# Kernel optimization log

Measured on AMD Instinct MI355X. Metric: run time of the kernel, lower is better.

The kernel has to match this reference:

```python
import jax, jax.numpy as jnp
import numpy as np

B = 16384          # batch
D = 1024           # input_size == hidden size of each block
L = 3              # number of hidden blocks (layer_configs)
H, Q = 4, 64       # num_heads, query_size
NKV, V = 128, 256  # num_key_values, value_size  (H*V == D for residual)
OUT = 256          # out_size
EPS = 1e-5


def layernorm(x, g, b):
    m = jnp.mean(x, axis=-1, keepdims=True)
    v = jnp.mean(jnp.square(x - m), axis=-1, keepdims=True)
    return (x - m) * jax.lax.rsqrt(v + EPS) * g + b


def setup_inputs() -> dict:
    key = jax.random.key(0)
    ks = jax.random.split(key, 16)
    scale = 1e-4  # module scales Linear / out_linear weights by 0.0001 at init
    return {
        "x": jax.random.normal(ks[0], (B, D), jnp.float32),
        # per-block Linear (stacked over L identical blocks)
        "W": jax.random.normal(ks[1], (L, D, D), jnp.float32) * scale / np.sqrt(D),
        "b": jax.random.normal(ks[2], (L, D), jnp.float32) * scale,
        # MemLayer params
        "Wq": jax.random.normal(ks[3], (L, H * Q, D), jnp.float32) / np.sqrt(D),
        "keys": jax.random.normal(ks[4], (L, NKV, Q), jnp.float32),
        "values": jax.random.normal(ks[5], (L, NKV, V), jnp.float32),
        "Wout": jax.random.normal(ks[6], (L, D, H * V), jnp.float32) * scale / np.sqrt(H * V),
        # per-block LayerNorm
        "ln_g": jnp.ones((L, D), jnp.float32),
        "ln_b": jnp.zeros((L, D), jnp.float32),
        # final head: Linear(sum(layer_configs)=L*D -> OUT), LayerNorm, Sigmoid
        "Wf": jax.random.normal(ks[7], (OUT, L * D), jnp.float32) * scale / np.sqrt(L * D),
        "bf": jax.random.normal(ks[8], (OUT,), jnp.float32) * scale,
        "lnf_g": jnp.ones((OUT,), jnp.float32),
        "lnf_b": jnp.zeros((OUT,), jnp.float32),
    }


def reference(x, W, b, Wq, keys, values, Wout, ln_g, ln_b, Wf, bf, lnf_g, lnf_b):
    # Dropout layers are identity at inference.
    inv_sqrt_q = 1.0 / np.sqrt(Q).astype(np.float32)
    outs = []
    h = x
    for i in range(L):
        # Linear + ReLU
        h = jax.nn.relu(h @ W[i].T + b[i])
        # MemLayer: scores = einsum('aib,ajb->aijb').sum(-1) == q @ k^T
        q = (h @ Wq[i].T).reshape(B, H, Q)
        scores = jnp.einsum('ahq,nq->ahn', q, keys[i]) * inv_sqrt_q  # (B,H,NKV)
        attn = jax.nn.softmax(scores, axis=-1)
        # einsum('aib,ajc->aijc').mean(axis=2) == attn.sum(-1)[:,:,None] * values.mean(0)
        s = jnp.sum(attn, axis=-1)              # (B,H)
        vmean = jnp.mean(values[i], axis=0)     # (V,)
        mem = (s[:, :, None] * vmean).reshape(B, H * V)
        h = mem @ Wout[i].T + h                 # out_linear + residual
        # LayerNorm (output collected for the final concat)
        h = layernorm(h, ln_g[i], ln_b[i])
        outs.append(h)
    z = jnp.concatenate(outs, axis=-1)          # (B, L*D)
    z = z @ Wf.T + bf
    z = layernorm(z, lnf_g, lnf_b)
    return jax.nn.sigmoid(z)
```

## Files before the change

### kernel.cpp

```cpp
#include <hip/hip_runtime.h>
#include <math.h>

#define EPS 1e-5f

constexpr int Bv   = 16384;
constexpr int Dv   = 1024;
constexpr int Lv   = 3;
constexpr int NKVv = 128;
constexpr int Vv   = 256;
constexpr int OUTv = 256;
constexpr int ZLD  = Lv * Dv;

typedef short bf16x8 __attribute__((ext_vector_type(8)));
typedef float f32x4  __attribute__((ext_vector_type(4)));

using gas_t = __attribute__((address_space(1))) const void;
using las_t = __attribute__((address_space(3))) void;
#define GLD_LDS16(gp, lp) \
    __builtin_amdgcn_global_load_lds((gas_t*)(gp), (las_t*)(lp), 16, 0, 0)

static __device__ __forceinline__ ushort f2bf(float f) {
    unsigned u = __float_as_uint(f);
    u = (u + 0x7fffu + ((u >> 16) & 1u)) >> 16;
    return (ushort)u;
}
static __device__ __forceinline__ ushort f2h(float f) {
    return __builtin_bit_cast(ushort, (_Float16)f);
}
static __device__ __forceinline__ float h2f(ushort u) {
    return (float)__builtin_bit_cast(_Float16, u);
}

__global__ void vmean_kernel(const float* __restrict__ values,
                             float* __restrict__ vmean) {
    const int i = blockIdx.x, t = threadIdx.x;
    const float* vals = values + (size_t)i * NKVv * Vv;
    float s = 0.f;
    for (int n = 0; n < NKVv; ++n) s += vals[n * Vv + t];
    vmean[i * Vv + t] = s * (1.0f / NKVv);
}

__global__ void cvec_kernel(const float* __restrict__ vmean,
                            const float* __restrict__ Wout,
                            float* __restrict__ cvec) {
    const int w = threadIdx.x >> 6, lane = threadIdx.x & 63;
    const int r = blockIdx.x * 8 + w;
    const int i = r >> 10;
    const float4 mv = *(const float4*)&vmean[i * Vv + lane * 4];
    const float* row = Wout + (size_t)r * 1024;
    float acc = 0.f;
#pragma unroll
    for (int c = 0; c < 4; ++c) {
        const float4 rv = *(const float4*)&row[c * 256 + lane * 4];
        acc += mv.x * rv.x + mv.y * rv.y + mv.z * rv.z + mv.w * rv.w;
    }
#pragma unroll
    for (int o = 1; o < 64; o <<= 1) acc += __shfl_xor(acc, o, 64);
    if (lane == 0) cvec[r] = acc;
}

__global__ void wprep(const float* __restrict__ W,
                      const float* __restrict__ lng,
                      const float* __restrict__ lnb,
                      ushort* __restrict__ Wb,
                      float* __restrict__ ub, float* __restrict__ vb) {
    __shared__ float rs[8];
    const int row = blockIdx.x;
    const int i = row >> 10, n = row & 1023;
    const int t = threadIdx.x, lane = t & 63, wv = t >> 6;
    const float* Wr = W + (size_t)row * 1024;
    const float4 w4 = *(const float4*)&Wr[t * 4];
    float4 g4 = make_float4(1.f, 1.f, 1.f, 1.f);
    float4 b4 = make_float4(0.f, 0.f, 0.f, 0.f);
    if (i > 0) {
        g4 = *(const float4*)&lng[(i - 1) * 1024 + t * 4];
        b4 = *(const float4*)&lnb[(i - 1) * 1024 + t * 4];
    }
    const float s0 = w4.x * g4.x, s1 = w4.y * g4.y, s2 = w4.z * g4.z, s3 = w4.w * g4.w;
    ushort4 o = {f2bf(s0), f2bf(s1), f2bf(s2), f2bf(s3)};
    *(ushort4*)&Wb[(size_t)row * 1024 + t * 4] = o;
    float su = s0 + s1 + s2 + s3;
    float sv = w4.x * b4.x + w4.y * b4.y + w4.z * b4.z + w4.w * b4.w;
#pragma unroll
    for (int d = 1; d < 64; d <<= 1) {
        su += __shfl_xor(su, d, 64);
        sv += __shfl_xor(sv, d, 64);
    }
    if (lane == 0) { rs[wv * 2] = su; rs[wv * 2 + 1] = sv; }
    __syncthreads();
    if (t == 0 && i > 0) {
        ub[(i - 1) * 1024 + n] = rs[0] + rs[2] + rs[4] + rs[6];
        vb[(i - 1) * 1024 + n] = rs[1] + rs[3] + rs[5] + rs[7];
    }
}

__global__ void wfprep(const float* __restrict__ Wf,
                       const float* __restrict__ lng,
                       const float* __restrict__ lnb,
                       ushort* __restrict__ Wfb,
                       float* __restrict__ uf, float* __restrict__ vf) {
    __shared__ float rs[8];
    const int bid = blockIdx.x;
    const int i = bid >> 8, n = bid & 255;
    const int t = threadIdx.x, lane = t & 63, wv = t >> 6;
    const size_t base = (size_t)n * ZLD + i * 1024 + t * 4;
    const float4 w4 = *(const float4*)&Wf[base];
    const float4 g4 = *(const float4*)&lng[i * 1024 + t * 4];
    const float4 b4 = *(const float4*)&lnb[i * 1024 + t * 4];
    const float s0 = w4.x * g4.x, s1 = w4.y * g4.y, s2 = w4.z * g4.z, s3 = w4.w * g4.w;
    ushort4 o = {f2bf(s0), f2bf(s1), f2bf(s2), f2bf(s3)};
    *(ushort4*)&Wfb[base] = o;
    float su = s0 + s1 + s2 + s3;
    float sv = w4.x * b4.x + w4.y * b4.y + w4.z * b4.z + w4.w * b4.w;
#pragma unroll
    for (int d = 1; d < 64; d <<= 1) {
        su += __shfl_xor(su, d, 64);
        sv += __shfl_xor(sv, d, 64);
    }
    if (lane == 0) { rs[wv * 2] = su; rs[wv * 2 + 1] = sv; }
    __syncthreads();
    if (t == 0) {
        uf[i * 256 + n] = rs[0] + rs[2] + rs[4] + rs[6];
        vf[i * 256 + n] = rs[1] + rs[3] + rs[5] + rs[7];
    }
}

__global__ void conv_x(const float* __restrict__ x, ushort* __restrict__ z) {
    const int t = blockIdx.x * 256 + threadIdx.x;
    const int row = t >> 7, c8 = (t & 127) << 3;
    const float4 v0 = *(const float4*)&x[(size_t)row * 1024 + c8];
    const float4 v1 = *(const float4*)&x[(size_t)row * 1024 + c8 + 4];
    ushort4 o0 = {f2bf(v0.x), f2bf(v0.y), f2bf(v0.z), f2bf(v0.w)};
    ushort4 o1 = {f2bf(v1.x), f2bf(v1.y), f2bf(v1.z), f2bf(v1.w)};
    ushort* p = z + (size_t)row * ZLD + 2048 + c8;
    *(ushort4*)p       = o0;
    *(ushort4*)(p + 4) = o1;
}

#define READ_A(QR, DD)                                                        \
    do { _Pragma("unroll")                                                    \
        for (int mf = 0; mf < 4; ++mf) {                                      \
            const int _o = (DD) * 16384 + (QR) * 8192 + (arow_l + mf * 16) * 64; \
            aR[mf][0] = *(const bf16x8*)&As[_o + ck0];                        \
            aR[mf][1] = *(const bf16x8*)&As[_o + ck1];                        \
        } } while (0)

#define READ_B(QC, DD, BR)                                                    \
    do { _Pragma("unroll")                                                    \
        for (int nf = 0; nf < 2; ++nf) {                                      \
            const int _o = (DD) * 16384 + (QC) * 8192 + (brow_l + nf * 16) * 64; \
            BR[nf][0] = *(const bf16x8*)&Bs[_o + ck0];                        \
            BR[nf][1] = *(const bf16x8*)&Bs[_o + ck1];                        \
        } } while (0)

#define STAGE_A(KT, H, DD)                                                    \
    do { const ushort* _p = gAs + (size_t)((H) * 128 + w16) * lda + (KT) * 64; \
         ushort* _l = As + (DD) * 16384 + (H) * 8192 + w16 * 64;              \
         GLD_LDS16(_p, _l);                                                   \
         GLD_LDS16(_p + (size_t)8 * lda, _l + 512); } while (0)

#define STAGE_B(KT, H, DD)                                                    \
    do { const ushort* _p = gBs + (size_t)((H) * 128 + w16) * ldb + (KT) * 64; \
         ushort* _l = Bs + (DD) * 16384 + (H) * 8192 + w16 * 64;              \
         GLD_LDS16(_p, _l);                                                   \
         GLD_LDS16(_p + (size_t)8 * ldb, _l + 512); } while (0)

#define MFMA_Q(QR, QC, BR)                                                    \
    do { __builtin_amdgcn_s_setprio(1);                                       \
        _Pragma("unroll")                                                     \
        for (int mf = 0; mf < 4; ++mf) {                                      \
            _Pragma("unroll")                                                 \
            for (int nf = 0; nf < 2; ++nf) {                                  \
                acc[QR][QC][mf][nf] = __builtin_amdgcn_mfma_f32_16x16x32_bf16( \
                    aR[mf][0], BR[nf][0], acc[QR][QC][mf][nf], 0, 0, 0);      \
                acc[QR][QC][mf][nf] = __builtin_amdgcn_mfma_f32_16x16x32_bf16( \
                    aR[mf][1], BR[nf][1], acc[QR][QC][mf][nf], 0, 0, 0);      \
            }                                                                 \
        }                                                                     \
        __builtin_amdgcn_s_setprio(0); } while (0)

template<int MODE>
__global__ __launch_bounds__(512, 1)
void gemm256(const ushort* __restrict__ A, int lda,
             const ushort* __restrict__ Bw, int ldb,
             const float* __restrict__ bias,
             const float* __restrict__ cvec,
             const float* __restrict__ u_,
             const float* __restrict__ v_,
             const float2* __restrict__ pstats_in,
             float2* __restrict__ mrout,
             void* __restrict__ Cv, int ldc,
             int NT, int ksplit,
             float2* __restrict__ pstats_out) {
    __shared__ __align__(16) char smem[139264];
    ushort* As = (ushort*)smem;
    ushort* Bs = (ushort*)(smem + 65536);
    float2* mrs = (float2*)(smem + 137216);
    const int tid  = threadIdx.x;
    const int lane = tid & 63;
    const int w    = tid >> 6;
    const int wr2  = w >> 2, wc2 = w & 3;
    const int w16  = w * 16;

    const int wg  = blockIdx.x;
    const int qchunk = (MODE == 1) ? 24 : 32;
    const int swz = (wg & 7) * qchunk + (wg >> 3);
    const int by  = swz & 63;
    const int bx  = swz >> 6;
    const int m0  = by * 256;
    const int n0  = (MODE == 1) ? 0 : bx * 256;
    const int koff = (MODE == 1) ? bx * ksplit : 0;

    const int swzc = ((lane & 7) ^ ((lane >> 3) & 7)) << 3;
    const ushort* gAs = A  + (size_t)(m0 + (lane >> 3)) * lda + koff + swzc;
    const ushort* gBs = Bw + (size_t)(n0 + (lane >> 3)) * ldb + koff + swzc;

    const int arow_l = wr2 * 64 + (lane & 15);
    const int brow_l = wc2 * 32 + (lane & 15);
    const int ck0 = (((lane >> 4))     ^ (lane & 7)) << 3;
    const int ck1 = ((4 + (lane >> 4)) ^ (lane & 7)) << 3;

    f32x4 acc[2][2][4][2] = {};
    bf16x8 aR[4][2], bR0[2][2], bR1[2][2];

    const bool doMR = (MODE == 2) || (MODE == 1 && bx == 2);
    float2 myMR = make_float2(0.f, 0.f);
    if (doMR && tid < 256) {
        const float4* pp = (const float4*)(pstats_in + (((size_t)(m0 + tid)) << 4));
        float sum = 0.f, sq = 0.f;
#pragma unroll
        for (int j = 0; j < 8; ++j) {
            const float4 t4 = pp[j];
            sum += t4.x + t4.z; sq += t4.y + t4.w;
        }
        const float m = sum * (1.f / Dv);
        const float var = sq * (1.f / Dv) - m * m;
        myMR = make_float2(m, rsqrtf(var + EPS));
        if (MODE == 2) mrs[tid] = myMR;
    }
    __builtin_amdgcn_sched_barrier(0);

    STAGE_A(0, 0, 0);
    STAGE_B(0, 0, 0);
    STAGE_B(0, 1, 0);
    STAGE_A(0, 1, 0);
    asm volatile("s_waitcnt vmcnt(4)" ::: "memory");
    __builtin_amdgcn_s_barrier();

    for (int t = 0; t < NT; ++t) {
        const int d  = t & 1;
        const int e2 = d ^ 1;
        const bool pf = (t + 1) < NT;
        READ_A(0, d);
        READ_B(0, d, bR0);
        if (pf) STAGE_A(t + 1, 0, e2);
        if (pf) asm volatile("s_waitcnt vmcnt(4)" ::: "memory");
        else    asm volatile("s_waitcnt vmcnt(2)" ::: "memory");
        __builtin_amdgcn_s_barrier();
        MFMA_Q(0, 0, bR0);
        READ_B(1, d, bR1);
        if (pf) STAGE_B(t + 1, 0, e2);
        if (pf) asm volatile("s_waitcnt vmcnt(4)" ::: "memory");
        else    asm volatile("s_waitcnt vmcnt(0)" ::: "memory");
        __builtin_amdgcn_s_barrier();
        MFMA_Q(0, 1, bR1);
        READ_A(1, d);
        if (pf) STAGE_B(t + 1, 1, e2);
        MFMA_Q(1, 1, bR1);
        if (pf) STAGE_A(t + 1, 1, e2);
        if (pf) asm volatile("s_waitcnt vmcnt(4)" ::: "memory");
        __builtin_amdgcn_s_barrier();
        MFMA_Q(1, 0, bR0);
    }

    if (doMR && tid < 256 && (MODE == 1 || bx == 0)) mrout[m0 + tid] = myMR;

    const int lg4 = (lane >> 4) << 2;
    ushort* tile = (ushort*)(smem + 2048);
    if (MODE != 1) {
        float bsv[2][2], csv[2][2], uu[2][2], vv[2][2];
#pragma unroll
        for (int qc = 0; qc < 2; ++qc)
#pragma unroll
            for (int nf = 0; nf < 2; ++nf) {
                const int col = n0 + qc * 128 + wc2 * 32 + nf * 16 + (lane & 15);
                bsv[qc][nf] = bias[col];
                csv[qc][nf] = cvec[col];
                if (MODE == 2) { uu[qc][nf] = u_[col]; vv[qc][nf] = v_[col]; }
            }
        __syncthreads();
#pragma unroll
        for (int qr = 0; qr < 2; ++qr)
#pragma unroll
            for (int mf = 0; mf < 4; ++mf)
#pragma unroll
                for (int r = 0; r < 4; ++r) {
                    const int rloc = qr * 128 + wr2 * 64 + mf * 16 + lg4 + r;
                    float rw = 1.f, rmw = 0.f;
                    if (MODE == 2) {
                        const float2 q = mrs[rloc];
                        rw = q.y; rmw = q.y * q.x;
                    }
                    float sum = 0.f, sq = 0.f;
#pragma unroll
                    for (int qc = 0; qc < 2; ++qc)
#pragma unroll
                        for (int nf = 0; nf < 2; ++nf) {
                            float a = acc[qr][qc][mf][nf][r];
                            float val;
                            if (MODE == 2)
                                val = fmaf(rw, a, fmaf(-rmw, uu[qc][nf],
                                          vv[qc][nf] + bsv[qc][nf]));
                            else
                                val = a + bsv[qc][nf];
                            val = fmaxf(val, 0.f) + csv[qc][nf];
                            acc[qr][qc][mf][nf][r] = val;
                            sum += val; sq += val * val;
                        }
#pragma unroll
                    for (int o = 1; o < 16; o <<= 1) {
                        sum += __shfl_xor(sum, o, 64);
                        sq  += __shfl_xor(sq,  o, 64);
                    }
                    if ((lane & 15) == 0)
                        pstats_out[(((size_t)(m0 + rloc)) << 4) + (bx << 2) + wc2] =
                            make_float2(sum, sq);
                }
#pragma unroll
        for (int qr = 0; qr < 2; ++qr)
#pragma unroll
            for (int qc = 0; qc < 2; ++qc)
#pragma unroll
                for (int mf = 0; mf < 4; ++mf)
#pragma unroll
                    for (int nf = 0; nf < 2; ++nf)
#pragma unroll
                        for (int r = 0; r < 4; ++r) {
                            const int rloc = qr * 128 + wr2 * 64 + mf * 16 + lg4 + r;
                            const int cloc = qc * 128 + wc2 * 32 + nf * 16 + (lane & 15);
                            tile[rloc * 264 + cloc] = f2bf(acc[qr][qc][mf][nf][r]);
                        }
    } else {
        __syncthreads();
#pragma unroll
        for (int qr = 0; qr < 2; ++qr)
#pragma unroll
            for (int qc = 0; qc < 2; ++qc)
#pragma unroll
                for (int mf = 0; mf < 4; ++mf)
#pragma unroll
                    for (int nf = 0; nf < 2; ++nf)
#pragma unroll
                        for (int r = 0; r < 4; ++r) {
                            const int rloc = qr * 128 + wr2 * 64 + mf * 16 + lg4 + r;
                            const int cloc = qc * 128 + wc2 * 32 + nf * 16 + (lane & 15);
                            tile[rloc * 264 + cloc] = f2h(acc[qr][qc][mf][nf][r]);
                        }
    }
    __syncthreads();
    ushort* C16 = (MODE == 1)
        ? ((ushort*)Cv + (size_t)bx * ((size_t)Bv * OUTv))
        : (ushort*)Cv;
    for (int c = tid; c < 256 * 32; c += 512) {
        const int row = c >> 5, ch = (c & 31) << 3;
        const bf16x8 v = *(const bf16x8*)&tile[row * 264 + ch];
        *(bf16x8*)&C16[(size_t)(m0 + row) * ldc + n0 + ch] = v;
    }
}

__global__ void ln_sig_reduce(const ushort* __restrict__ ps,
                              const float2* __restrict__ mr,
                              const float* __restrict__ uf,
                              const float* __restrict__ vf,
                              const float* __restrict__ bf_,
                              const float* __restrict__ g,
                              const float* __restrict__ bb,
                              float* __restrict__ y) {
    const int lane = threadIdx.x & 63;
    const int row  = blockIdx.x * 4 + (threadIdx.x >> 6);
    const size_t base = (size_t)row * OUTv + lane * 4;
    const size_t SP = (size_t)Bv * OUTv;
    const float2 q0 = mr[row];
    const float2 q1 = mr[Bv + row];
    const float2 q2 = mr[2 * Bv + row];
    const ushort4 a0 = *(const ushort4*)&ps[base];
    const ushort4 a1 = *(const ushort4*)&ps[base + SP];
    const ushort4 a2 = *(const ushort4*)&ps[base + 2 * SP];
    const float4 u0 = *(const float4*)&uf[lane * 4];
    const float4 u1 = *(const float4*)&uf[256 + lane * 4];
    const float4 u2 = *(const float4*)&uf[512 + lane * 4];
    const float4 f0 = *(const float4*)&vf[lane * 4];
    const float4 f1 = *(const float4*)&vf[256 + lane * 4];
    const float4 f2 = *(const float4*)&vf[512 + lane * 4];
    const float4 bv4 = *(const float4*)&bf_[lane * 4];
    const float cst_x = f0.x + f1.x + f2.x + bv4.x;
    const float cst_y = f0.y + f1.y + f2.y + bv4.y;
    const float cst_z = f0.z + f1.z + f2.z + bv4.z;
    const float cst_w = f0.w + f1.w + f2.w + bv4.w;
    const float v0 = q0.y * (h2f(a0.x) - q0.x * u0.x) + q1.y * (h2f(a1.x) - q1.x * u1.x)
                   + q2.y * (h2f(a2.x) - q2.x * u2.x) + cst_x;
    const float v1 = q0.y * (h2f(a0.y) - q0.x * u0.y) + q1.y * (h2f(a1.y) - q1.x * u1.y)
                   + q2.y * (h2f(a2.y) - q2.x * u2.y) + cst_y;
    const float v2 = q0.y * (h2f(a0.z) - q0.x * u0.z) + q1.y * (h2f(a1.z) - q1.x * u1.z)
                   + q2.y * (h2f(a2.z) - q2.x * u2.z) + cst_z;
    const float v3 = q0.y * (h2f(a0.w) - q0.x * u0.w) + q1.y * (h2f(a1.w) - q1.x * u1.w)
                   + q2.y * (h2f(a2.w) - q2.x * u2.w) + cst_w;
    float s = v0 + v1 + v2 + v3;
#pragma unroll
    for (int o = 1; o < 64; o <<= 1) s += __shfl_xor(s, o, 64);
    const float mean = s * (1.f / OUTv);
    const float d0 = v0 - mean, d1 = v1 - mean, d2 = v2 - mean, d3 = v3 - mean;
    float q = d0 * d0 + d1 * d1 + d2 * d2 + d3 * d3;
#pragma unroll
    for (int o = 1; o < 64; o <<= 1) q += __shfl_xor(q, o, 64);
    const float r = rsqrtf(q * (1.f / OUTv) + EPS);
    const float4 gg = *(const float4*)&g[lane * 4];
    const float4 bv = *(const float4*)&bb[lane * 4];
    float4 o;
    const float t0 = d0 * r * gg.x + bv.x;
    const float t1 = d1 * r * gg.y + bv.y;
    const float t2 = d2 * r * gg.z + bv.z;
    const float t3 = d3 * r * gg.w + bv.w;
    o.x = 1.f / (1.f + expf(-t0));
    o.y = 1.f / (1.f + expf(-t1));
    o.z = 1.f / (1.f + expf(-t2));
    o.w = 1.f / (1.f + expf(-t3));
    *(float4*)&y[base] = o;
}

extern "C" void kernel_launch(void* const* d_in, const int* in_sizes, int n_in,
                              void* d_out, int out_size, void* d_ws, size_t ws_size,
                              hipStream_t stream) {
    const float* x      = (const float*)d_in[0];
    const float* W      = (const float*)d_in[1];
    const float* b      = (const float*)d_in[2];
    const float* values = (const float*)d_in[5];
    const float* Wout   = (const float*)d_in[6];
    const float* ln_g   = (const float*)d_in[7];
    const float* ln_b   = (const float*)d_in[8];
    const float* Wf     = (const float*)d_in[9];
    const float* bf     = (const float*)d_in[10];
    const float* lnf_g  = (const float*)d_in[11];
    const float* lnf_b  = (const float*)d_in[12];
    float* out = (float*)d_out;

    char* ws = (char*)d_ws;
    ushort* zbuf = (ushort*)ws;
    ws += (size_t)Bv * ZLD * sizeof(ushort);
    ushort* psum = (ushort*)ws;
    ws += (size_t)3 * Bv * OUTv * sizeof(ushort);
    ushort* Wb = (ushort*)ws;
    ws += (size_t)Lv * Dv * Dv * sizeof(ushort);
    ushort* Wfb = (ushort*)ws;
    ws += (size_t)OUTv * ZLD * sizeof(ushort);
    float* cvec = (float*)ws;
    ws += (size_t)Lv * Dv * sizeof(float);
    float* vmean = (float*)ws;
    ws += (size_t)Lv * Vv * sizeof(float);
    float2* psA = (float2*)ws;
    ws += (size_t)Bv * 16 * sizeof(float2);
    float2* psB = (float2*)ws;
    ws += (size_t)Bv * 16 * sizeof(float2);
    float2* mr3 = (float2*)ws;
    ws += (size_t)3 * Bv * sizeof(float2);
    float* ub = (float*)ws; ws += 2 * Dv * sizeof(float);
    float* vb = (float*)ws; ws += 2 * Dv * sizeof(float);
    float* uf = (float*)ws; ws += 3 * OUTv * sizeof(float);
    float* vf = (float*)ws; ws += 3 * OUTv * sizeof(float);

    wprep<<<Lv * Dv, 256, 0, stream>>>(W, ln_g, ln_b, Wb, ub, vb);
    wfprep<<<3 * OUTv, 256, 0, stream>>>(Wf, ln_g, ln_b, Wfb, uf, vf);
    conv_x<<<Bv * 128 / 256, 256, 0, stream>>>(x, zbuf);
    vmean_kernel<<<Lv, 256, 0, stream>>>(values, vmean);
    cvec_kernel<<<Lv * Dv / 8, 512, 0, stream>>>(vmean, Wout, cvec);

    gemm256<0><<<dim3(256), 512, 0, stream>>>(
        zbuf + 2048, ZLD, Wb, Dv,
        b, cvec, nullptr, nullptr, nullptr, nullptr,
        (void*)(zbuf + 0), ZLD, 16, 0, psA);

    gemm256<2><<<dim3(256), 512, 0, stream>>>(
        zbuf, ZLD, Wb + (size_t)Dv * Dv, Dv,
        b + Dv, cvec + Dv, ub, vb, psA, mr3,
        (void*)(zbuf + Dv), ZLD, 16, 0, psB);

    gemm256<2><<<dim3(256), 512, 0, stream>>>(
        zbuf + Dv, ZLD, Wb + (size_t)2 * Dv * Dv, Dv,
        b + 2 * Dv, cvec + 2 * Dv, ub + Dv, vb + Dv, psB, mr3 + Bv,
        (void*)(zbuf + 2 * Dv), ZLD, 16, 0, psA);

    gemm256<1><<<dim3(192), 512, 0, stream>>>(
        zbuf, ZLD, Wfb, ZLD, nullptr, nullptr, nullptr, nullptr,
        psA, mr3 + 2 * Bv,
        (void*)psum, OUTv, 16, 1024, nullptr);

    ln_sig_reduce<<<Bv / 4, 256, 0, stream>>>(psum, mr3, uf, vf, bf,
                                              lnf_g, lnf_b, out);
}
```

Measured before the change: 205.2 us.

## Deepen GEMM prefetch pipeline and remap workgroup tile order

Restructures the LDS staging schedule so global loads for A and B tiles are issued about two iterations ahead instead of one. The prologue now stages part of the next tile, and each quarter-step is fenced with extra barriers and adjusted vmcnt waits. For non-split modes it also changes the workgroup-to-tile mapping so groups of 8 row blocks share a column block, which is meant to improve L2 reuse. The extra barriers add synchronization cost, and reusing the double buffer this far ahead makes correctness depend on exact barrier placement.

```diff
diff --git a/kernel.cpp b/kernel.cpp
--- a/kernel.cpp
+++ b/kernel.cpp
@@ -203,10 +203,15 @@
     const int w16  = w * 16;
 
     const int wg  = blockIdx.x;
-    const int qchunk = (MODE == 1) ? 24 : 32;
-    const int swz = (wg & 7) * qchunk + (wg >> 3);
-    const int by  = swz & 63;
-    const int bx  = swz >> 6;
+    int by, bx;
+    if (MODE == 1) {
+        const int swz = (wg & 7) * 24 + (wg >> 3);
+        by = swz & 63; bx = swz >> 6;
+    } else {
+        const int j = wg >> 3;
+        by = (wg & 7) * 8 + (j & 7);
+        bx = j >> 3;
+    }
     const int m0  = by * 256;
     const int n0  = (MODE == 1) ? 0 : bx * 256;
     const int koff = (MODE == 1) ? bx * ksplit : 0;
@@ -244,33 +249,37 @@
     STAGE_B(0, 0, 0);
     STAGE_B(0, 1, 0);
     STAGE_A(0, 1, 0);
-    asm volatile("s_waitcnt vmcnt(4)" ::: "memory");
+    STAGE_A(1, 0, 1);
+    STAGE_B(1, 0, 1);
+    STAGE_B(1, 1, 1);
+    asm volatile("s_waitcnt vmcnt(6)" ::: "memory");
     __builtin_amdgcn_s_barrier();
 
     for (int t = 0; t < NT; ++t) {
         const int d  = t & 1;
         const int e2 = d ^ 1;
-        const bool pf = (t + 1) < NT;
         READ_A(0, d);
         READ_B(0, d, bR0);
-        if (pf) STAGE_A(t + 1, 0, e2);
-        if (pf) asm volatile("s_waitcnt vmcnt(4)" ::: "memory");
-        else    asm volatile("s_waitcnt vmcnt(2)" ::: "memory");
+        if (t + 1 < NT) STAGE_A(t + 1, 1, e2);
         __builtin_amdgcn_s_barrier();
         MFMA_Q(0, 0, bR0);
+        __builtin_amdgcn_s_barrier();
         READ_B(1, d, bR1);
-        if (pf) STAGE_B(t + 1, 0, e2);
-        if (pf) asm volatile("s_waitcnt vmcnt(4)" ::: "memory");
-        else    asm volatile("s_waitcnt vmcnt(0)" ::: "memory");
+        if (t + 2 < NT) STAGE_A(t + 2, 0, d);
         __builtin_amdgcn_s_barrier();
         MFMA_Q(0, 1, bR1);
+        __builtin_amdgcn_s_barrier();
         READ_A(1, d);
-        if (pf) STAGE_B(t + 1, 1, e2);
+        if (t + 2 < NT) STAGE_B(t + 2, 0, d);
+        __builtin_amdgcn_s_barrier();
         MFMA_Q(1, 1, bR1);
-        if (pf) STAGE_A(t + 1, 1, e2);
-        if (pf) asm volatile("s_waitcnt vmcnt(4)" ::: "memory");
+        __builtin_amdgcn_s_barrier();
+        if (t + 2 < NT) STAGE_B(t + 2, 1, d);
+        if (t + 2 < NT)      asm volatile("s_waitcnt vmcnt(6)" ::: "memory");
+        else if (t + 1 < NT) asm volatile("s_waitcnt vmcnt(0)" ::: "memory");
         __builtin_amdgcn_s_barrier();
         MFMA_Q(1, 0, bR0);
+        __builtin_amdgcn_s_barrier();
     }
 
     if (doMR && tid < 256 && (MODE == 1 || bx == 0)) mrout[m0 + tid] = myMR;
```

New measurement: 213.5 us. +4.0%, slower.
